# Kernel optimization log

Hardware: AMD Instinct MI355X
Metric: run time of the kernel (lower is better)

Reference implementation:

```python
import jax, jax.numpy as jnp
import numpy as np

H = 16  # heads


def setup_inputs() -> dict:
    key = jax.random.key(0)
    ks = jax.random.split(key, 10)
    B, S, M = 4, 2048, 1024
    scale = 1.0 / np.sqrt(M)
    return {
        "x": jax.random.normal(ks[0], (B, S, M), dtype=jnp.float32),
        "mask": jax.random.uniform(ks[1], (B, 1, S, S), dtype=jnp.float32),
        "Wq": jax.random.normal(ks[2], (M, M), dtype=jnp.float32) * scale,
        "bq": jax.random.normal(ks[3], (M,), dtype=jnp.float32) * scale,
        "Wk": jax.random.normal(ks[4], (M, M), dtype=jnp.float32) * scale,
        "bk": jax.random.normal(ks[5], (M,), dtype=jnp.float32) * scale,
        "Wv": jax.random.normal(ks[6], (M, M), dtype=jnp.float32) * scale,
        "bv": jax.random.normal(ks[7], (M,), dtype=jnp.float32) * scale,
        "Wo": jax.random.normal(ks[8], (M, M), dtype=jnp.float32) * scale,
        "bo": jax.random.normal(ks[9], (M,), dtype=jnp.float32) * scale,
    }


def reference(x, mask, Wq, bq, Wk, bk, Wv, bv, Wo, bo):
    B, S, M = x.shape
    dk = M // H
    # QKV projections (torch Linear: x @ W.T + b), then split heads -> [B,H,S,dk]
    q = (x @ Wq.T + bq).reshape(B, S, H, dk).transpose(0, 2, 1, 3)
    k = (x @ Wk.T + bk).reshape(B, S, H, dk).transpose(0, 2, 1, 3)
    v = (x @ Wv.T + bv).reshape(B, S, H, dk).transpose(0, 2, 1, 3)
    # scores: [B,H,S,S], multiplicative mask (non-standard!) then softmax
    scores = jnp.einsum("bhqd,bhkd->bhqk", q, k) / jnp.sqrt(jnp.float32(dk))
    scores = scores * mask  # mask broadcasts over heads
    attn = jax.nn.softmax(scores, axis=-1)
    # dropout is identity in eval/reference mode
    out = jnp.einsum("bhqk,bhkd->bhqd", attn, v)  # [B,H,S,dk]
    concat = out.transpose(0, 2, 1, 3).reshape(B, S, M)
    return concat @ Wo.T + bo
```

## Files before the change

kernel.cpp:

```cpp
#include <hip/hip_runtime.h>

typedef __attribute__((ext_vector_type(8))) short s16x8;
typedef __attribute__((ext_vector_type(4))) short s16x4;
typedef __attribute__((ext_vector_type(4))) float f32x4;
typedef __attribute__((ext_vector_type(2))) float f32x2;
typedef __attribute__((ext_vector_type(16))) float f32x16;
typedef __attribute__((ext_vector_type(2))) unsigned int u32x2;

#define DEV static __device__ __forceinline__

DEV void gload_lds16(const void* g, void* l) {
  __builtin_amdgcn_global_load_lds(
      (const __attribute__((address_space(1))) void*)g,
      (__attribute__((address_space(3))) void*)l, 16, 0, 0);
}

DEV unsigned short f2bf(float f) {
  unsigned int u = __float_as_uint(f);
  u = (u + 0x7fffu + ((u >> 16) & 1u)) >> 16;
  return (unsigned short)u;
}

DEV unsigned pk2(float lo, float hi) {
  unsigned r;
  asm("v_cvt_pk_bf16_f32 %0, %1, %2" : "=v"(r) : "v"(lo), "v"(hi));
  return r;
}

DEV float exp2_fast(float x) {
  float r;
  asm("v_exp_f32 %0, %1" : "=v"(r) : "v"(x));
  return r;
}

DEV f32x2 pk_mul(f32x2 a, f32x2 b) {
  f32x2 d;
  asm("v_pk_mul_f32 %0, %1, %2" : "=v"(d) : "v"(a), "v"(b));
  return d;
}

DEV f32x2 pk_add(f32x2 a, f32x2 b) {
  f32x2 d;
  asm("v_pk_add_f32 %0, %1, %2" : "=v"(d) : "v"(a), "v"(b));
  return d;
}

DEV float swap32_add(float x) {
  const u32x2 r = __builtin_amdgcn_permlane32_swap(__float_as_uint(x), __float_as_uint(x),
                                                   false, false);
  return __uint_as_float(r.x) + __uint_as_float(r.y);
}

DEV void cvt8(const float* __restrict__ in, unsigned short* __restrict__ out, int i) {
  float4 a = *(const float4*)(in + i);
  float4 b = *(const float4*)(in + i + 4);
  union { s16x8 v; unsigned short u[8]; } o;
  o.u[0] = f2bf(a.x); o.u[1] = f2bf(a.y); o.u[2] = f2bf(a.z); o.u[3] = f2bf(a.w);
  o.u[4] = f2bf(b.x); o.u[5] = f2bf(b.y); o.u[6] = f2bf(b.z); o.u[7] = f2bf(b.w);
  *(s16x8*)(out + i) = o.v;
}

__global__ __launch_bounds__(256) void k_prep(
    const float* __restrict__ x, const float* __restrict__ mask,
    const float* __restrict__ Wq, const float* __restrict__ Wk,
    const float* __restrict__ Wv, const float* __restrict__ Wo,
    unsigned short* __restrict__ xb, unsigned short* __restrict__ wcat,
    unsigned short* __restrict__ slab) {
  __shared__ unsigned short Mt[128 * 68];
  const int bid = blockIdx.x;
  const int tid = threadIdx.x;
  if (bid < 4096) {
    cvt8(x, xb, (bid * 256 + tid) * 8);
    return;
  }
  if (bid < 6144) {
    const int id = bid - 4096;
    const int sel = id >> 9;
    const float* in = (sel == 0) ? Wq : (sel == 1) ? Wk : (sel == 2) ? Wv : Wo;
    cvt8(in, wcat + sel * 1048576, ((id & 511) * 256 + tid) * 8);
    return;
  }
  const int id = bid - 6144;
  const int t = id & 31, qt = (id >> 5) & 15, b = id >> 9;
  const float* src = mask + (size_t)b * 4194304 + (size_t)qt * 128 * 2048 + t * 64;
#pragma unroll
  for (int it = 0; it < 8; ++it) {
    const int c = it * 256 + tid;
    const int row = c >> 4, kc = c & 15;
    const float4 v = *(const float4*)(src + (size_t)row * 2048 + kc * 4);
    unsigned short* d = Mt + row * 68 + kc * 4;
    d[0] = f2bf(v.x); d[1] = f2bf(v.y); d[2] = f2bf(v.z); d[3] = f2bf(v.w);
  }
  __syncthreads();
  unsigned short* dst = slab + ((((size_t)b * 16 + qt) * 32 + t) * 8192);
#pragma unroll
  for (int it = 0; it < 4; ++it) {
    const int c = it * 256 + tid;
    const int w = c >> 8, i2 = (c >> 6) & 3, ln = c & 63;
    const int qrow = w * 32 + (ln & 31);
    const int kbase = 32 * (i2 >> 1) + 16 * (i2 & 1) + 4 * (ln >> 5);
    union { s16x8 v; unsigned short u[8]; } o;
#pragma unroll
    for (int e = 0; e < 8; ++e)
      o.u[e] = Mt[qrow * 68 + kbase + 8 * (e >> 2) + (e & 3)];
    *(s16x8*)(dst + c * 8) = o.v;
  }
}

__global__ __launch_bounds__(256) void k_gemm_qkv(
    const unsigned short* __restrict__ A, const unsigned short* __restrict__ Bcat,
    const float* __restrict__ bq, const float* __restrict__ bk,
    const float* __restrict__ bv,
    unsigned short* __restrict__ outQK, unsigned short* __restrict__ vtw) {
  constexpr int K = 1024;
  constexpr float QSC = 0.125f * 1.44269504f;
  __shared__ unsigned short As[128 * 64];
  __shared__ unsigned short Bs[128 * 64];

  const int lin = blockIdx.x;
  const int logical = (lin & 7) * 192 + (lin >> 3);
  const int nb = logical % 24;
  const int mb = logical / 24;
  const int m0 = mb * 128;
  const int n0 = nb * 128;
  const int z = n0 >> 10;

  const int tid = threadIdx.x;
  const int lane = tid & 63;
  const int l15 = lane & 15, g = lane >> 4;
  const int w = tid >> 6;
  const int wr = w >> 1, wc = w & 1;

  const int sr = tid >> 3;
  const int sc = tid & 7;

  f32x4 acc[4][4] = {};

  for (int kt = 0; kt < K / 64; ++kt) {
#pragma unroll
    for (int i = 0; i < 4; ++i) {
      const int row = i * 32 + sr;
      gload_lds16(A + (size_t)(m0 + row) * K + kt * 64 + ((sc ^ (row & 7)) * 8),
                  (void*)(As + i * 2048 + tid * 8));
      gload_lds16(Bcat + (size_t)(n0 + row) * K + kt * 64 + ((sc ^ (row & 7)) * 8),
                  (void*)(Bs + i * 2048 + tid * 8));
    }
    __syncthreads();
#pragma unroll
    for (int ks = 0; ks < 2; ++ks) {
      s16x8 af[4], bf[4];
#pragma unroll
      for (int i = 0; i < 4; ++i) {
        const int ra = wr * 64 + i * 16 + l15;
        af[i] = *(const s16x8*)(As + ra * 64 + (((ks * 4 + g) ^ (ra & 7)) * 8));
        const int rb = wc * 64 + i * 16 + l15;
        bf[i] = *(const s16x8*)(Bs + rb * 64 + (((ks * 4 + g) ^ (rb & 7)) * 8));
      }
#pragma unroll
      for (int i = 0; i < 4; ++i)
#pragma unroll
        for (int j = 0; j < 4; ++j)
          acc[i][j] = __builtin_amdgcn_mfma_f32_16x16x32_bf16(af[i], bf[j], acc[i][j], 0, 0, 0);
    }
    __syncthreads();
  }

  const float* bias = (z == 0) ? bq : (z == 1) ? bk : bv;
  const float osc = (z == 0) ? QSC : 1.0f;
#pragma unroll
  for (int j = 0; j < 4; ++j) {
    const int gcol = n0 + wc * 64 + j * 16 + l15;
    const int col = gcol & 1023;
    const float bvv = bias[col];
    const int h = col >> 6, d = col & 63;
#pragma unroll
    for (int i = 0; i < 4; ++i) {
      const int grow0 = m0 + wr * 64 + i * 16 + g * 4;
      const int bb = grow0 >> 11, s0 = grow0 & 2047;
      if (z < 2) {
        unsigned short* outp = outQK + (size_t)z * 8388608;
#pragma unroll
        for (int r = 0; r < 4; ++r)
          outp[(((size_t)(bb * 16 + h) * 2048 + (s0 + r)) << 6) + d] =
              f2bf((acc[i][j][r] + bvv) * osc);
      } else {
        union { s16x4 v; unsigned short u[4]; } pk;
#pragma unroll
        for (int r = 0; r < 4; ++r) pk.u[r] = f2bf(acc[i][j][r] + bvv);
        *(s16x4*)(vtw + (((size_t)(bb * 16 + h)) << 17) + (size_t)d * 2048 + s0) = pk.v;
      }
    }
  }
}

__global__ __launch_bounds__(256) void k_gemm_o(
    const unsigned short* __restrict__ A, const unsigned short* __restrict__ Bw,
    const float* __restrict__ bias, float* __restrict__ outp) {
  constexpr int K = 1024;
  __shared__ unsigned short As[128 * 64];
  __shared__ unsigned short Bs[64 * 64];

  const int lin = blockIdx.x;
  const int logical = (lin & 7) * 128 + (lin >> 3);
  const int nb = logical & 15;
  const int mb = logical >> 4;
  const int m0 = mb * 128, n0 = nb * 64;

  const int tid = threadIdx.x;
  const int lane = tid & 63;
  const int l15 = lane & 15, g = lane >> 4;
  const int w = tid >> 6;
  const int wr = w >> 1, wc = w & 1;

  const int sr = tid >> 3;
  const int sc = tid & 7;

  f32x4 acc[4][2] = {};

  for (int kt = 0; kt < K / 64; ++kt) {
#pragma unroll
    for (int i = 0; i < 4; ++i) {
      const int row = i * 32 + sr;
      gload_lds16(A + (size_t)(m0 + row) * K + kt * 64 + ((sc ^ (row & 7)) * 8),
                  (void*)(As + i * 2048 + tid * 8));
    }
#pragma unroll
    for (int i = 0; i < 2; ++i) {
      const int row = i * 32 + sr;
      gload_lds16(Bw + (size_t)(n0 + row) * K + kt * 64 + ((sc ^ (row & 7)) * 8),
                  (void*)(Bs + i * 2048 + tid * 8));
    }
    __syncthreads();
#pragma unroll
    for (int ks = 0; ks < 2; ++ks) {
      s16x8 af[4], bf[2];
#pragma unroll
      for (int mi = 0; mi < 4; ++mi) {
        const int ra = wr * 64 + mi * 16 + l15;
        af[mi] = *(const s16x8*)(As + ra * 64 + (((ks * 4 + g) ^ (ra & 7)) * 8));
      }
#pragma unroll
      for (int nj = 0; nj < 2; ++nj) {
        const int rb = wc * 32 + nj * 16 + l15;
        bf[nj] = *(const s16x8*)(Bs + rb * 64 + (((ks * 4 + g) ^ (rb & 7)) * 8));
      }
#pragma unroll
      for (int mi = 0; mi < 4; ++mi)
#pragma unroll
        for (int nj = 0; nj < 2; ++nj)
          acc[mi][nj] =
              __builtin_amdgcn_mfma_f32_16x16x32_bf16(af[mi], bf[nj], acc[mi][nj], 0, 0, 0);
    }
    __syncthreads();
  }

#pragma unroll
  for (int nj = 0; nj < 2; ++nj) {
    const int gcol = n0 + wc * 32 + nj * 16 + l15;
    const float bv = bias[gcol];
#pragma unroll
    for (int mi = 0; mi < 4; ++mi)
#pragma unroll
      for (int r = 0; r < 4; ++r) {
        const int grow = m0 + wr * 64 + mi * 16 + g * 4 + r;
        outp[(size_t)grow * 1024 + gcol] = acc[mi][nj][r] + bv;
      }
  }
}

__global__ __launch_bounds__(256) void k_attn6(
    const unsigned short* __restrict__ q, const unsigned short* __restrict__ k,
    const unsigned short* __restrict__ vt, const unsigned short* __restrict__ slab,
    unsigned short* __restrict__ concat) {
  __shared__ unsigned short Ks[2][64 * 64];
  __shared__ unsigned short Vs[2][64 * 64];

  const int tid = threadIdx.x;
  const int lane = tid & 63;
  const int w = tid >> 6;
  const int l31 = lane & 31;
  const int hh = lane >> 5;

  const int lin = blockIdx.x + 16 * (blockIdx.y + 16 * blockIdx.z);
  const int logical = (lin & 7) * 128 + (lin >> 3);
  const int h = logical & 15;
  const int qt = (logical >> 4) & 15;
  const int b = logical >> 8;

  const size_t bhO = (size_t)(b * 16 + h) * (2048 * 64);
  const unsigned short* kb = k + bhO;
  const unsigned short* vb = vt + bhO;
  const int q0 = qt * 128;
  const int qc = w * 32 + l31;
  const int qg = q0 + qc;

  s16x8 qf[4];
  {
    const unsigned short* qp = q + bhO + (size_t)qg * 64 + hh * 8;
#pragma unroll
    for (int kd = 0; kd < 4; ++kd) qf[kd] = *(const s16x8*)(qp + kd * 16);
  }

  const unsigned short* mp =
      slab + ((((size_t)b * 16 + qt) * 32) * 8192) + ((size_t)(w * 4) * 64 + lane) * 8;

  float l_r = 0.f;
  f32x16 oacc[2] = {};

  const int sr = tid >> 3;
  const int sc = tid & 7;

#define STAGE(BUF, T_)                                                                \
  {                                                                                   \
    const int kv0s = (T_)*64;                                                         \
    _Pragma("unroll") for (int i = 0; i < 2; ++i) {                                   \
      const int row = i * 32 + sr;                                                    \
      const int sz = (sc ^ (row & 7)) * 8;                                            \
      gload_lds16(kb + (size_t)(kv0s + row) * 64 + sz,                                \
                  (void*)(Ks[BUF] + i * 2048 + tid * 8));                             \
      gload_lds16(vb + (size_t)row * 2048 + kv0s + sz,                                \
                  (void*)(Vs[BUF] + i * 2048 + tid * 8));                             \
    }                                                                                 \
  }

  STAGE(0, 0)
  __syncthreads();

  for (int tt = 0; tt < 16; ++tt) {
#pragma unroll
    for (int half = 0; half < 2; ++half) {
      const int t = tt * 2 + half;

      s16x8 mv[4];
#pragma unroll
      for (int i2 = 0; i2 < 4; ++i2) mv[i2] = *(const s16x8*)(mp + i2 * 512);
      mp += 8192;

      if (t < 31) STAGE(half ^ 1, t + 1)

      f32x16 sacc[2] = {};
      __builtin_amdgcn_s_setprio(1);
#pragma unroll
      for (int f = 0; f < 2; ++f) {
        const int rk = f * 32 + l31;
        const unsigned short* Kr = Ks[half] + rk * 64;
        const int swb = rk & 7;
#pragma unroll
        for (int kd = 0; kd < 4; ++kd) {
          const s16x8 kf = *(const s16x8*)(Kr + (((kd * 2 + hh) ^ swb) * 8));
          sacc[f] = __builtin_amdgcn_mfma_f32_32x32x16_bf16(kf, qf[kd], sacc[f], 0, 0, 0);
        }
      }
      __builtin_amdgcn_s_setprio(0);

      f32x2 u[16];
#pragma unroll
      for (int f = 0; f < 2; ++f)
#pragma unroll
        for (int kk = 0; kk < 2; ++kk) {
          union { s16x8 v; unsigned d[4]; } mw;
          mw.v = mv[f * 2 + kk];
#pragma unroll
          for (int d = 0; d < 4; ++d) {
            const unsigned m = mw.d[d];
            f32x2 mpv, sp;
            mpv.x = __uint_as_float(m << 16);
            mpv.y = __uint_as_float(m & 0xffff0000u);
            sp.x = sacc[f][kk * 8 + d * 2];
            sp.y = sacc[f][kk * 8 + d * 2 + 1];
            u[f * 8 + kk * 4 + d] = pk_mul(sp, mpv);
          }
        }
#pragma unroll
      for (int j = 0; j < 16; ++j) {
        u[j].x = exp2_fast(u[j].x);
        u[j].y = exp2_fast(u[j].y);
      }

      f32x2 t8[8];
#pragma unroll
      for (int j = 0; j < 8; ++j) t8[j] = pk_add(u[2 * j], u[2 * j + 1]);
      f32x2 t4[4];
#pragma unroll
      for (int j = 0; j < 4; ++j) t4[j] = pk_add(t8[2 * j], t8[2 * j + 1]);
      const f32x2 t2a = pk_add(t4[0], t4[1]);
      const f32x2 t2b = pk_add(t4[2], t4[3]);
      const f32x2 t1 = pk_add(t2a, t2b);
      l_r += swap32_add(t1.x + t1.y);

#pragma unroll
      for (int ks = 0; ks < 4; ++ks) {
        const unsigned X0 = pk2(u[ks * 4 + 0].x, u[ks * 4 + 0].y);
        const unsigned X1 = pk2(u[ks * 4 + 1].x, u[ks * 4 + 1].y);
        const unsigned Y0 = pk2(u[ks * 4 + 2].x, u[ks * 4 + 2].y);
        const unsigned Y1 = pk2(u[ks * 4 + 3].x, u[ks * 4 + 3].y);
        const u32x2 r0 = __builtin_amdgcn_permlane32_swap(X0, Y0, false, false);
        const u32x2 r1 = __builtin_amdgcn_permlane32_swap(X1, Y1, false, false);
        union { s16x8 v; unsigned u[4]; } pf;
        pf.u[0] = r0.x; pf.u[1] = r1.x; pf.u[2] = r0.y; pf.u[3] = r1.y;
        __builtin_amdgcn_s_setprio(1);
#pragma unroll
        for (int df = 0; df < 2; ++df) {
          const int rv = df * 32 + l31;
          const s16x8 vf =
              *(const s16x8*)(Vs[half] + rv * 64 + (((ks * 2 + hh) ^ (rv & 7)) * 8));
          oacc[df] = __builtin_amdgcn_mfma_f32_32x32x16_bf16(vf, pf.v, oacc[df], 0, 0, 0);
        }
        __builtin_amdgcn_s_setprio(0);
      }
      __syncthreads();
    }
  }
#undef STAGE

  const float inv = 1.0f / l_r;
  unsigned short* cb = concat + ((size_t)b * 2048 + qg) * 1024 + h * 64;
#pragma unroll
  for (int df = 0; df < 2; ++df)
#pragma unroll
    for (int r = 0; r < 16; r += 2) {
      const int d = df * 32 + (r & 3) + 8 * (r >> 2) + 4 * hh;
      const unsigned uo = (unsigned)f2bf(oacc[df][r] * inv) |
                          ((unsigned)f2bf(oacc[df][r + 1] * inv) << 16);
      *(unsigned*)(cb + d) = uo;
    }
}

extern "C" void kernel_launch(void* const* d_in, const int* in_sizes, int n_in,
                              void* d_out, int out_size, void* d_ws, size_t ws_size,
                              hipStream_t stream) {
  const float* x    = (const float*)d_in[0];
  const float* mask = (const float*)d_in[1];
  const float* Wq   = (const float*)d_in[2];
  const float* bq   = (const float*)d_in[3];
  const float* Wk   = (const float*)d_in[4];
  const float* bk   = (const float*)d_in[5];
  const float* Wv   = (const float*)d_in[6];
  const float* bv   = (const float*)d_in[7];
  const float* Wo   = (const float*)d_in[8];
  const float* bo   = (const float*)d_in[9];

  char* ws = (char*)d_ws;
  unsigned short* xb    = (unsigned short*)(ws);
  unsigned short* wcat  = (unsigned short*)(ws + (size_t)16777216);
  unsigned short* wob   = wcat + 3 * 1048576;
  unsigned short* qw    = (unsigned short*)(ws + (size_t)25165824);
  unsigned short* kw    = qw + 8388608;
  unsigned short* vtw   = (unsigned short*)(ws + (size_t)58720256);
  unsigned short* slab  = (unsigned short*)(ws + (size_t)75497472);
  unsigned short* cw    = xb;

  k_prep<<<dim3(8192), dim3(256), 0, stream>>>(x, mask, Wq, Wk, Wv, Wo, xb, wcat, slab);
  k_gemm_qkv<<<dim3(1536), dim3(256), 0, stream>>>(xb, wcat, bq, bk, bv, qw, vtw);
  k_attn6<<<dim3(16, 16, 4), dim3(256), 0, stream>>>(qw, kw, vtw, slab, cw);
  k_gemm_o<<<dim3(1024), dim3(256), 0, stream>>>(cw, wob, bo, (float*)d_out);
}
```

Baseline: 228.8 us.

## Load K/V fragments directly into registers, drop LDS staging and barriers

The attention kernel no longer stages K and V tiles through double-buffered shared memory with __syncthreads. Each wave now loads its K, V and mask fragments straight from global memory into registers and prefetches the next tile while the current one computes. This removes the LDS traffic and block barriers, at the cost of redundant global/L2 reads across the four waves, more register pressure, and less coalesced loads. The prep kernel also replaces eight scalar shared-memory reads with two 4-wide vector reads when building the mask slab.

```diff
diff --git a/kernel.cpp b/kernel.cpp
--- a/kernel.cpp
+++ b/kernel.cpp
@@ -99,10 +99,9 @@
     const int w = c >> 8, i2 = (c >> 6) & 3, ln = c & 63;
     const int qrow = w * 32 + (ln & 31);
     const int kbase = 32 * (i2 >> 1) + 16 * (i2 & 1) + 4 * (ln >> 5);
-    union { s16x8 v; unsigned short u[8]; } o;
-#pragma unroll
-    for (int e = 0; e < 8; ++e)
-      o.u[e] = Mt[qrow * 68 + kbase + 8 * (e >> 2) + (e & 3)];
+    union { s16x8 v; s16x4 h[2]; } o;
+    o.h[0] = *(const s16x4*)(Mt + qrow * 68 + kbase);
+    o.h[1] = *(const s16x4*)(Mt + qrow * 68 + kbase + 8);
     *(s16x8*)(dst + c * 8) = o.v;
   }
 }
@@ -268,13 +267,10 @@
   }
 }
 
-__global__ __launch_bounds__(256) void k_attn6(
+__global__ __launch_bounds__(256) void k_attn8(
     const unsigned short* __restrict__ q, const unsigned short* __restrict__ k,
     const unsigned short* __restrict__ vt, const unsigned short* __restrict__ slab,
     unsigned short* __restrict__ concat) {
-  __shared__ unsigned short Ks[2][64 * 64];
-  __shared__ unsigned short Vs[2][64 * 64];
-
   const int tid = threadIdx.x;
   const int lane = tid & 63;
   const int w = tid >> 6;
@@ -288,8 +284,6 @@
   const int b = logical >> 8;
 
   const size_t bhO = (size_t)(b * 16 + h) * (2048 * 64);
-  const unsigned short* kb = k + bhO;
-  const unsigned short* vb = vt + bhO;
   const int q0 = qt * 128;
   const int qc = w * 32 + l31;
   const int qg = q0 + qc;
@@ -301,82 +295,76 @@
     for (int kd = 0; kd < 4; ++kd) qf[kd] = *(const s16x8*)(qp + kd * 16);
   }
 
+  const unsigned short* kp = k + bhO + (size_t)l31 * 64 + hh * 8;
+  const unsigned short* vp = vt + bhO + (size_t)l31 * 2048 + hh * 8;
   const unsigned short* mp =
       slab + ((((size_t)b * 16 + qt) * 32) * 8192) + ((size_t)(w * 4) * 64 + lane) * 8;
 
   float l_r = 0.f;
   f32x16 oacc[2] = {};
 
-  const int sr = tid >> 3;
-  const int sc = tid & 7;
-
-#define STAGE(BUF, T_)                                                                \
-  {                                                                                   \
-    const int kv0s = (T_)*64;                                                         \
-    _Pragma("unroll") for (int i = 0; i < 2; ++i) {                                   \
-      const int row = i * 32 + sr;                                                    \
-      const int sz = (sc ^ (row & 7)) * 8;                                            \
-      gload_lds16(kb + (size_t)(kv0s + row) * 64 + sz,                                \
-                  (void*)(Ks[BUF] + i * 2048 + tid * 8));                             \
-      gload_lds16(vb + (size_t)row * 2048 + kv0s + sz,                                \
-                  (void*)(Vs[BUF] + i * 2048 + tid * 8));                             \
-    }                                                                                 \
-  }
-
-  STAGE(0, 0)
-  __syncthreads();
-
-  for (int tt = 0; tt < 16; ++tt) {
-#pragma unroll
-    for (int half = 0; half < 2; ++half) {
-      const int t = tt * 2 + half;
-
-      s16x8 mv[4];
-#pragma unroll
-      for (int i2 = 0; i2 < 4; ++i2) mv[i2] = *(const s16x8*)(mp + i2 * 512);
-      mp += 8192;
-
-      if (t < 31) STAGE(half ^ 1, t + 1)
-
-      f32x16 sacc[2] = {};
-      __builtin_amdgcn_s_setprio(1);
-#pragma unroll
-      for (int f = 0; f < 2; ++f) {
-        const int rk = f * 32 + l31;
-        const unsigned short* Kr = Ks[half] + rk * 64;
-        const int swb = rk & 7;
-#pragma unroll
-        for (int kd = 0; kd < 4; ++kd) {
-          const s16x8 kf = *(const s16x8*)(Kr + (((kd * 2 + hh) ^ swb) * 8));
-          sacc[f] = __builtin_amdgcn_mfma_f32_32x32x16_bf16(kf, qf[kd], sacc[f], 0, 0, 0);
+  s16x8 kf[2][4], vf[2][4], mv[4];
+#pragma unroll
+  for (int f = 0; f < 2; ++f)
+#pragma unroll
+    for (int c = 0; c < 4; ++c) {
+      kf[f][c] = *(const s16x8*)(kp + f * 2048 + c * 16);
+      vf[f][c] = *(const s16x8*)(vp + (size_t)f * 65536 + c * 16);
+    }
+#pragma unroll
+  for (int i2 = 0; i2 < 4; ++i2) mv[i2] = *(const s16x8*)(mp + i2 * 512);
+
+  for (int t = 0; t < 32; ++t) {
+    f32x16 sacc[2] = {};
+    __builtin_amdgcn_s_setprio(1);
+#pragma unroll
+    for (int f = 0; f < 2; ++f)
+#pragma unroll
+      for (int kd = 0; kd < 4; ++kd)
+        sacc[f] = __builtin_amdgcn_mfma_f32_32x32x16_bf16(kf[f][kd], qf[kd], sacc[f], 0, 0, 0);
+    __builtin_amdgcn_s_setprio(0);
+
+    {
+      const unsigned short* kpn = kp + (size_t)((t + 1) & 31) * 4096;
+#pragma unroll
+      for (int f = 0; f < 2; ++f)
+#pragma unroll
+        for (int kd = 0; kd < 4; ++kd)
+          kf[f][kd] = *(const s16x8*)(kpn + f * 2048 + kd * 16);
+    }
+
+    f32x2 u[16];
+#pragma unroll
+    for (int f = 0; f < 2; ++f)
+#pragma unroll
+      for (int kk = 0; kk < 2; ++kk) {
+        union { s16x8 v; unsigned d[4]; } mw;
+        mw.v = mv[f * 2 + kk];
+#pragma unroll
+        for (int d = 0; d < 4; ++d) {
+          const unsigned m = mw.d[d];
+          f32x2 mpv, sp;
+          mpv.x = __uint_as_float(m << 16);
+          mpv.y = __uint_as_float(m & 0xffff0000u);
+          sp.x = sacc[f][kk * 8 + d * 2];
+          sp.y = sacc[f][kk * 8 + d * 2 + 1];
+          u[f * 8 + kk * 4 + d] = pk_mul(sp, mpv);
         }
       }
-      __builtin_amdgcn_s_setprio(0);
-
-      f32x2 u[16];
-#pragma unroll
-      for (int f = 0; f < 2; ++f)
-#pragma unroll
-        for (int kk = 0; kk < 2; ++kk) {
-          union { s16x8 v; unsigned d[4]; } mw;
-          mw.v = mv[f * 2 + kk];
-#pragma unroll
-          for (int d = 0; d < 4; ++d) {
-            const unsigned m = mw.d[d];
-            f32x2 mpv, sp;
-            mpv.x = __uint_as_float(m << 16);
-            mpv.y = __uint_as_float(m & 0xffff0000u);
-            sp.x = sacc[f][kk * 8 + d * 2];
-            sp.y = sacc[f][kk * 8 + d * 2 + 1];
-            u[f * 8 + kk * 4 + d] = pk_mul(sp, mpv);
-          }
-        }
-#pragma unroll
-      for (int j = 0; j < 16; ++j) {
-        u[j].x = exp2_fast(u[j].x);
-        u[j].y = exp2_fast(u[j].y);
-      }
-
+
+    {
+      const unsigned short* mpn = mp + (size_t)((t + 1) & 31) * 8192;
+#pragma unroll
+      for (int i2 = 0; i2 < 4; ++i2) mv[i2] = *(const s16x8*)(mpn + i2 * 512);
+    }
+
+#pragma unroll
+    for (int j = 0; j < 16; ++j) {
+      u[j].x = exp2_fast(u[j].x);
+      u[j].y = exp2_fast(u[j].y);
+    }
+
+    {
       f32x2 t8[8];
 #pragma unroll
       for (int j = 0; j < 8; ++j) t8[j] = pk_add(u[2 * j], u[2 * j + 1]);
@@ -387,31 +375,34 @@
       const f32x2 t2b = pk_add(t4[2], t4[3]);
       const f32x2 t1 = pk_add(t2a, t2b);
       l_r += swap32_add(t1.x + t1.y);
-
-#pragma unroll
-      for (int ks = 0; ks < 4; ++ks) {
-        const unsigned X0 = pk2(u[ks * 4 + 0].x, u[ks * 4 + 0].y);
-        const unsigned X1 = pk2(u[ks * 4 + 1].x, u[ks * 4 + 1].y);
-        const unsigned Y0 = pk2(u[ks * 4 + 2].x, u[ks * 4 + 2].y);
-        const unsigned Y1 = pk2(u[ks * 4 + 3].x, u[ks * 4 + 3].y);
-        const u32x2 r0 = __builtin_amdgcn_permlane32_swap(X0, Y0, false, false);
-        const u32x2 r1 = __builtin_amdgcn_permlane32_swap(X1, Y1, false, false);
-        union { s16x8 v; unsigned u[4]; } pf;
-        pf.u[0] = r0.x; pf.u[1] = r1.x; pf.u[2] = r0.y; pf.u[3] = r1.y;
-        __builtin_amdgcn_s_setprio(1);
-#pragma unroll
-        for (int df = 0; df < 2; ++df) {
-          const int rv = df * 32 + l31;
-          const s16x8 vf =
-              *(const s16x8*)(Vs[half] + rv * 64 + (((ks * 2 + hh) ^ (rv & 7)) * 8));
-          oacc[df] = __builtin_amdgcn_mfma_f32_32x32x16_bf16(vf, pf.v, oacc[df], 0, 0, 0);
-        }
-        __builtin_amdgcn_s_setprio(0);
-      }
-      __syncthreads();
-    }
-  }
-#undef STAGE
+    }
+
+#pragma unroll
+    for (int ks = 0; ks < 4; ++ks) {
+      const unsigned X0 = pk2(u[ks * 4 + 0].x, u[ks * 4 + 0].y);
+      const unsigned X1 = pk2(u[ks * 4 + 1].x, u[ks * 4 + 1].y);
+      const unsigned Y0 = pk2(u[ks * 4 + 2].x, u[ks * 4 + 2].y);
+      const unsigned Y1 = pk2(u[ks * 4 + 3].x, u[ks * 4 + 3].y);
+      const u32x2 r0 = __builtin_amdgcn_permlane32_swap(X0, Y0, false, false);
+      const u32x2 r1 = __builtin_amdgcn_permlane32_swap(X1, Y1, false, false);
+      union { s16x8 v; unsigned u[4]; } pf;
+      pf.u[0] = r0.x; pf.u[1] = r1.x; pf.u[2] = r0.y; pf.u[3] = r1.y;
+      __builtin_amdgcn_s_setprio(1);
+#pragma unroll
+      for (int df = 0; df < 2; ++df)
+        oacc[df] = __builtin_amdgcn_mfma_f32_32x32x16_bf16(vf[df][ks], pf.v, oacc[df], 0, 0, 0);
+      __builtin_amdgcn_s_setprio(0);
+    }
+
+    {
+      const unsigned short* vpn = vp + (size_t)((t + 1) & 31) * 64;
+#pragma unroll
+      for (int df = 0; df < 2; ++df)
+#pragma unroll
+        for (int ks = 0; ks < 4; ++ks)
+          vf[df][ks] = *(const s16x8*)(vpn + (size_t)df * 65536 + ks * 16);
+    }
+  }
 
   const float inv = 1.0f / l_r;
   unsigned short* cb = concat + ((size_t)b * 2048 + qg) * 1024 + h * 64;
@@ -452,6 +443,6 @@
 
   k_prep<<<dim3(8192), dim3(256), 0, stream>>>(x, mask, Wq, Wk, Wv, Wo, xb, wcat, slab);
   k_gemm_qkv<<<dim3(1536), dim3(256), 0, stream>>>(xb, wcat, bq, bk, bv, qw, vtw);
-  k_attn6<<<dim3(16, 16, 4), dim3(256), 0, stream>>>(qw, kw, vtw, slab, cw);
+  k_attn8<<<dim3(16, 16, 4), dim3(256), 0, stream>>>(qw, kw, vtw, slab, cw);
   k_gemm_o<<<dim3(1024), dim3(256), 0, stream>>>(cw, wob, bo, (float*)d_out);
 }
```

New measurement: 363.2 us. 58.7% more time.

## Grow attention blocks to 512 threads sharing K/V tiles across two query tiles

Applied to the files above, without the earlier changes.

The attention kernel now runs 512-thread blocks, each covering two 128-row query tiles, so every staged K/V tile in LDS feeds eight waves instead of four. Each thread issues one K and one V async load per stage instead of two, which halves global K/V traffic per query row. The mask-prep kernel also reads LDS with two 8-byte vector loads instead of eight scalar loads. The cost is half as many blocks and a wider barrier per iteration, which may reduce latency hiding and occupancy flexibility.

```diff
diff --git a/kernel.cpp b/kernel.cpp
--- a/kernel.cpp
+++ b/kernel.cpp
@@ -99,10 +99,9 @@
     const int w = c >> 8, i2 = (c >> 6) & 3, ln = c & 63;
     const int qrow = w * 32 + (ln & 31);
     const int kbase = 32 * (i2 >> 1) + 16 * (i2 & 1) + 4 * (ln >> 5);
-    union { s16x8 v; unsigned short u[8]; } o;
-#pragma unroll
-    for (int e = 0; e < 8; ++e)
-      o.u[e] = Mt[qrow * 68 + kbase + 8 * (e >> 2) + (e & 3)];
+    union { s16x8 v; s16x4 h[2]; } o;
+    o.h[0] = *(const s16x4*)(Mt + qrow * 68 + kbase);
+    o.h[1] = *(const s16x4*)(Mt + qrow * 68 + kbase + 8);
     *(s16x8*)(dst + c * 8) = o.v;
   }
 }
@@ -268,7 +267,7 @@
   }
 }
 
-__global__ __launch_bounds__(256) void k_attn6(
+__global__ __launch_bounds__(512) void k_attn9(
     const unsigned short* __restrict__ q, const unsigned short* __restrict__ k,
     const unsigned short* __restrict__ vt, const unsigned short* __restrict__ slab,
     unsigned short* __restrict__ concat) {
@@ -278,21 +277,21 @@
   const int tid = threadIdx.x;
   const int lane = tid & 63;
   const int w = tid >> 6;
+  const int ww = w & 3;
   const int l31 = lane & 31;
   const int hh = lane >> 5;
 
-  const int lin = blockIdx.x + 16 * (blockIdx.y + 16 * blockIdx.z);
-  const int logical = (lin & 7) * 128 + (lin >> 3);
+  const int lin = blockIdx.x + 16 * (blockIdx.y + 8 * blockIdx.z);
+  const int logical = (lin & 7) * 64 + (lin >> 3);
   const int h = logical & 15;
-  const int qt = (logical >> 4) & 15;
-  const int b = logical >> 8;
+  const int qtb = (logical >> 4) & 7;
+  const int b = logical >> 7;
+  const int qt128 = qtb * 2 + (w >> 2);
 
   const size_t bhO = (size_t)(b * 16 + h) * (2048 * 64);
   const unsigned short* kb = k + bhO;
   const unsigned short* vb = vt + bhO;
-  const int q0 = qt * 128;
-  const int qc = w * 32 + l31;
-  const int qg = q0 + qc;
+  const int qg = qt128 * 128 + ww * 32 + l31;
 
   s16x8 qf[4];
   {
@@ -302,25 +301,20 @@
   }
 
   const unsigned short* mp =
-      slab + ((((size_t)b * 16 + qt) * 32) * 8192) + ((size_t)(w * 4) * 64 + lane) * 8;
+      slab + ((((size_t)b * 16 + qt128) * 32) * 8192) + ((size_t)(ww * 4) * 64 + lane) * 8;
 
   float l_r = 0.f;
   f32x16 oacc[2] = {};
 
-  const int sr = tid >> 3;
+  const int srow = tid >> 3;
   const int sc = tid & 7;
 
 #define STAGE(BUF, T_)                                                                \
   {                                                                                   \
     const int kv0s = (T_)*64;                                                         \
-    _Pragma("unroll") for (int i = 0; i < 2; ++i) {                                   \
-      const int row = i * 32 + sr;                                                    \
-      const int sz = (sc ^ (row & 7)) * 8;                                            \
-      gload_lds16(kb + (size_t)(kv0s + row) * 64 + sz,                                \
-                  (void*)(Ks[BUF] + i * 2048 + tid * 8));                             \
-      gload_lds16(vb + (size_t)row * 2048 + kv0s + sz,                                \
-                  (void*)(Vs[BUF] + i * 2048 + tid * 8));                             \
-    }                                                                                 \
+    const int sz = (sc ^ (srow & 7)) * 8;                                             \
+    gload_lds16(kb + (size_t)(kv0s + srow) * 64 + sz, (void*)(Ks[BUF] + tid * 8));    \
+    gload_lds16(vb + (size_t)srow * 2048 + kv0s + sz, (void*)(Vs[BUF] + tid * 8));    \
   }
 
   STAGE(0, 0)
@@ -377,16 +371,18 @@
         u[j].y = exp2_fast(u[j].y);
       }
 
-      f32x2 t8[8];
-#pragma unroll
-      for (int j = 0; j < 8; ++j) t8[j] = pk_add(u[2 * j], u[2 * j + 1]);
-      f32x2 t4[4];
-#pragma unroll
-      for (int j = 0; j < 4; ++j) t4[j] = pk_add(t8[2 * j], t8[2 * j + 1]);
-      const f32x2 t2a = pk_add(t4[0], t4[1]);
-      const f32x2 t2b = pk_add(t4[2], t4[3]);
-      const f32x2 t1 = pk_add(t2a, t2b);
-      l_r += swap32_add(t1.x + t1.y);
+      {
+        f32x2 t8[8];
+#pragma unroll
+        for (int j = 0; j < 8; ++j) t8[j] = pk_add(u[2 * j], u[2 * j + 1]);
+        f32x2 t4[4];
+#pragma unroll
+        for (int j = 0; j < 4; ++j) t4[j] = pk_add(t8[2 * j], t8[2 * j + 1]);
+        const f32x2 t2a = pk_add(t4[0], t4[1]);
+        const f32x2 t2b = pk_add(t4[2], t4[3]);
+        const f32x2 t1 = pk_add(t2a, t2b);
+        l_r += swap32_add(t1.x + t1.y);
+      }
 
 #pragma unroll
       for (int ks = 0; ks < 4; ++ks) {
@@ -452,6 +448,6 @@
 
   k_prep<<<dim3(8192), dim3(256), 0, stream>>>(x, mask, Wq, Wk, Wv, Wo, xb, wcat, slab);
   k_gemm_qkv<<<dim3(1536), dim3(256), 0, stream>>>(xb, wcat, bq, bk, bv, qw, vtw);
-  k_attn6<<<dim3(16, 16, 4), dim3(256), 0, stream>>>(qw, kw, vtw, slab, cw);
+  k_attn9<<<dim3(16, 8, 4), dim3(512), 0, stream>>>(qw, kw, vtw, slab, cw);
   k_gemm_o<<<dim3(1024), dim3(256), 0, stream>>>(cw, wob, bo, (float*)d_out);
 }
```

Measured after the change: 232.1 us. About the same (+1.4%).
